# Optimization experiments

Hardware: AMD Instinct MI355X
Metric: run time of the kernel (lower is better)

Reference implementation:

```python
import jax, jax.numpy as jnp
import numpy as np

C_Z = 128
C_HIDDEN = 128
N_RES = 384
B = 1
EPS = 1e-5


def _layernorm(x, w, b):
    mu = jnp.mean(x, axis=-1, keepdims=True)
    var = jnp.mean(jnp.square(x - mu), axis=-1, keepdims=True)
    return (x - mu) * jax.lax.rsqrt(var + EPS) * w + b


def setup_inputs() -> dict:
    key = jax.random.key(0)
    ks = jax.random.split(key, 16)
    s_z = 1.0 / np.sqrt(C_Z)
    s_h = 1.0 / np.sqrt(C_HIDDEN)
    return {
        "z": jax.random.normal(ks[0], (B, N_RES, N_RES, C_Z), dtype=jnp.float32),
        "mask": jnp.ones((B, N_RES, N_RES), dtype=jnp.float32),
        "ln_in_w": jnp.ones((C_Z,), jnp.float32),
        "ln_in_b": jnp.zeros((C_Z,), jnp.float32),
        "a_g_w": jax.random.normal(ks[1], (C_HIDDEN, C_Z), jnp.float32) * s_z,
        "a_g_b": jnp.zeros((C_HIDDEN,), jnp.float32),
        "a_p_w": jax.random.normal(ks[2], (C_HIDDEN, C_Z), jnp.float32) * s_z,
        "a_p_b": jnp.zeros((C_HIDDEN,), jnp.float32),
        "b_g_w": jax.random.normal(ks[3], (C_HIDDEN, C_Z), jnp.float32) * s_z,
        "b_g_b": jnp.zeros((C_HIDDEN,), jnp.float32),
        "b_p_w": jax.random.normal(ks[4], (C_HIDDEN, C_Z), jnp.float32) * s_z,
        "b_p_b": jnp.zeros((C_HIDDEN,), jnp.float32),
        "g_w": jax.random.normal(ks[5], (C_Z, C_Z), jnp.float32) * s_z,
        "g_b": jnp.zeros((C_Z,), jnp.float32),
        "ln_out_w": jnp.ones((C_HIDDEN,), jnp.float32),
        "ln_out_b": jnp.zeros((C_HIDDEN,), jnp.float32),
        "z_w": jax.random.normal(ks[6], (C_Z, C_HIDDEN), jnp.float32) * s_h,
        "z_b": jnp.zeros((C_Z,), jnp.float32),
    }


def reference(z, mask, ln_in_w, ln_in_b, a_g_w, a_g_b, a_p_w, a_p_b,
              b_g_w, b_g_b, b_p_w, b_p_b, g_w, g_b,
              ln_out_w, ln_out_b, z_w, z_b):
    # z: [B, N, N, c_z]; mask: [B, N, N]
    m = mask[..., None]
    zn = _layernorm(z, ln_in_w, ln_in_b)
    # gated projections (fused LN+GEMM+sigmoid*mul in the Triton kernel)
    a = m * jax.nn.sigmoid(jnp.einsum("bijc,hc->bijh", zn, a_g_w) + a_g_b) \
          * (jnp.einsum("bijc,hc->bijh", zn, a_p_w) + a_p_b)
    b = m * jax.nn.sigmoid(jnp.einsum("bijc,hc->bijh", zn, b_g_w) + b_g_b) \
          * (jnp.einsum("bijc,hc->bijh", zn, b_p_w) + b_p_b)
    # outgoing triangle update: contract over third node k, per channel
    x = jnp.einsum("bikh,bjkh->bijh", a, b)
    # output path: sigmoid(gate(zn)) * linear_z(LN_out(x))
    xn = _layernorm(x, ln_out_w, ln_out_b)
    gate = jax.nn.sigmoid(jnp.einsum("bijc,oc->bijo", zn, g_w) + g_b)
    out = gate * (jnp.einsum("bijh,oh->bijo", xn, z_w) + z_b)
    return out
```

## Files before the change

kernel.cpp:

```cpp
#include <hip/hip_runtime.h>

#define NRES 384
#define CD   128
#define MTOT (NRES*NRES)

typedef unsigned short u16;
typedef __bf16 bf16x8 __attribute__((ext_vector_type(8)));
typedef float  f32x16 __attribute__((ext_vector_type(16)));

static __device__ __forceinline__ u16 f2bf(float f) {
  __bf16 b = (__bf16)f;
  return __builtin_bit_cast(u16, b);
}
static __device__ __forceinline__ float bf2f(u16 v) {
  return __uint_as_float(((unsigned)v) << 16);
}
static __device__ __forceinline__ float sigmoidf(float x) {
  return __builtin_amdgcn_rcpf(1.0f + __expf(-x));
}

static __device__ __forceinline__ void gl16(const void* g, void* l) {
  __builtin_amdgcn_global_load_lds(
      (const __attribute__((address_space(1))) void*)g,
      (__attribute__((address_space(3))) void*)l, 16, 0, 0);
}

__global__ void k_cvt_w(const float* w0, const float* w1, const float* w2,
                        const float* w3, const float* w4, const float* w5,
                        const float* lnw, u16* wb) {
  int i = blockIdx.x * 256 + threadIdx.x;
  int which = blockIdx.x >> 6;
  const float* src = (which == 0) ? w0 : (which == 1) ? w1 : (which == 2) ? w2
                   : (which == 3) ? w3 : (which == 4) ? w4 : w5;
  float v = src[i & 16383];
  if (which == 5) v *= lnw[i & 127];
  wb[i] = f2bf(v);
}

__global__ void k_c12(const float* __restrict__ zw, const float* __restrict__ lnw,
                      const float* __restrict__ lnb, const float* __restrict__ zb,
                      float2* __restrict__ c12) {
  int o = blockIdx.x, l = threadIdx.x;
  float2 v = ((const float2*)(zw + o * CD))[l];
  float2 w = ((const float2*)lnw)[l];
  float2 b = ((const float2*)lnb)[l];
  float s1 = v.x * w.x + v.y * w.y;
  float s2 = v.x * b.x + v.y * b.y;
#pragma unroll
  for (int off = 32; off >= 1; off >>= 1) {
    s1 += __shfl_xor(s1, off);
    s2 += __shfl_xor(s2, off);
  }
  if (l == 0) c12[o] = make_float2(s1, s2 + zb[o]);
}

__global__ __launch_bounds__(256) void k_ln_in(const float* __restrict__ z,
                                               const float* __restrict__ w,
                                               const float* __restrict__ b,
                                               u16* __restrict__ zn) {
  int wv = threadIdx.x >> 6, lane = threadIdx.x & 63;
  float2 wv2 = ((const float2*)w)[lane];
  float2 bv2 = ((const float2*)b)[lane];
  for (int rr = 0; rr < 4; ++rr) {
    size_t row = (size_t)blockIdx.x * 16 + wv * 4 + rr;
    float2 v = ((const float2*)(z + row * CD))[lane];
    float s = v.x + v.y;
#pragma unroll
    for (int off = 32; off >= 1; off >>= 1) s += __shfl_xor(s, off);
    float mu = s * (1.0f / CD);
    float dx = v.x - mu, dy = v.y - mu;
    float vr = dx * dx + dy * dy;
#pragma unroll
    for (int off = 32; off >= 1; off >>= 1) vr += __shfl_xor(vr, off);
    float rs = rsqrtf(vr * (1.0f / CD) + 1e-5f);
    ushort2 o;
    o.x = f2bf(dx * rs * wv2.x + bv2.x);
    o.y = f2bf(dy * rs * wv2.y + bv2.y);
    ((ushort2*)(zn + row * CD))[lane] = o;
  }
}

__global__ __launch_bounds__(256) void k_proj(
    const u16* __restrict__ zn, const float* __restrict__ mask,
    const u16* __restrict__ wb,
    const float* __restrict__ agb, const float* __restrict__ apb,
    const float* __restrict__ bgb, const float* __restrict__ bpb,
    u16* __restrict__ a_out, u16* __restrict__ b_out) {
  int type = blockIdx.y;
  int m_base = blockIdx.x * 256;
  int t = threadIdx.x;
  int lane = t & 63;
  int wvu = __builtin_amdgcn_readfirstlane(t >> 6);
  int nl = lane & 31, s = lane >> 5;
  int h = wvu * 32 + nl;

  const u16* wgp = wb + (size_t)type * 32768;
  const u16* wpp = wgp + 16384;
  const float* bgp = (type == 0) ? agb : bgb;
  const float* bpp = (type == 0) ? apb : bpb;
  u16* outp = (type == 0) ? a_out : b_out;

  __shared__ u16 znt[3][64][128];
  __shared__ float bsl[2][128];

  if (t < 128) bsl[0][t] = bgp[t];
  else         bsl[1][t - 128] = bpp[t - 128];

  float mk0[4], mk1[4];
#pragma unroll
  for (int ms = 0; ms < 4; ++ms) {
    mk0[ms] = mask[m_base + ms * 64 + nl];
    mk1[ms] = mask[m_base + ms * 64 + 32 + nl];
  }

  bf16x8 wgf[8], wpf[8];
#pragma unroll
  for (int kk = 0; kk < 8; ++kk) {
    wgf[kk] = *(const bf16x8*)(wgp + h * CD + kk * 16 + s * 8);
    wpf[kk] = *(const bf16x8*)(wpp + h * CD + kk * 16 + s * 8);
  }

  int rl = lane >> 4, p16 = lane & 15;
#define STAGE_ZNT(mt, bf)                                                   \
  {                                                                         \
    _Pragma("unroll")                                                       \
    for (int j = 0; j < 4; ++j) {                                           \
      int row = wvu * 16 + j * 4 + rl;                                      \
      int gc = (p16 ^ (row & 15)) << 3;                                     \
      gl16(zn + (size_t)((mt) + row) * CD + gc, &znt[bf][wvu * 16 + j * 4][0]); \
    }                                                                       \
  }

  asm volatile("" ::: "memory");
  STAGE_ZNT(m_base, 0);
  asm volatile("" ::: "memory");
  STAGE_ZNT(m_base + 64, 1);
  asm volatile("" ::: "memory");

  asm volatile("s_waitcnt lgkmcnt(0)" ::: "memory");

#define PROJ_ITER(ms, buf, WAITINSN, STAGEIT, stbuf)                          \
  {                                                                           \
    asm volatile(WAITINSN ::: "memory");                                      \
    __builtin_amdgcn_s_barrier();                                             \
    asm volatile("" ::: "memory");                                            \
    f32x16 accg0, accg1, accp0, accp1;                                        \
    _Pragma("unroll")                                                         \
    for (int i = 0; i < 16; ++i) {                                            \
      accg0[i] = 0; accg1[i] = 0; accp0[i] = 0; accp1[i] = 0;                 \
    }                                                                         \
    _Pragma("unroll")                                                         \
    for (int kk = 0; kk < 8; ++kk) {                                          \
      int c = ((kk * 2 + s) ^ (nl & 15)) << 3;                                \
      bf16x8 zf0 = *(const bf16x8*)&znt[buf][nl][c];                          \
      bf16x8 zf1 = *(const bf16x8*)&znt[buf][32 + nl][c];                     \
      accg0 = __builtin_amdgcn_mfma_f32_32x32x16_bf16(wgf[kk], zf0, accg0, 0, 0, 0); \
      accg1 = __builtin_amdgcn_mfma_f32_32x32x16_bf16(wgf[kk], zf1, accg1, 0, 0, 0); \
      accp0 = __builtin_amdgcn_mfma_f32_32x32x16_bf16(wpf[kk], zf0, accp0, 0, 0, 0); \
      accp1 = __builtin_amdgcn_mfma_f32_32x32x16_bf16(wpf[kk], zf1, accp1, 0, 0, 0); \
    }                                                                         \
    int mt = m_base + (ms) * 64;                                              \
    _Pragma("unroll")                                                         \
    for (int r = 0; r < 16; ++r) {                                            \
      int hh = wvu * 32 + (r & 3) + 8 * (r >> 2) + 4 * s;                     \
      float bg = bsl[0][hh], bp = bsl[1][hh];                                 \
      u16* rowp = outp + (size_t)hh * MTOT + mt + nl;                         \
      rowp[0]  = f2bf(mk0[ms] * sigmoidf(accg0[r] + bg) * (accp0[r] + bp));   \
      rowp[32] = f2bf(mk1[ms] * sigmoidf(accg1[r] + bg) * (accp1[r] + bp));   \
    }                                                                         \
    asm volatile("" ::: "memory");                                            \
    if (STAGEIT) STAGE_ZNT(m_base + ((ms) + 2) * 64, stbuf);                  \
    asm volatile("" ::: "memory");                                            \
  }

  PROJ_ITER(0, 0, "s_waitcnt vmcnt(4)",  1, 2);
  PROJ_ITER(1, 1, "s_waitcnt vmcnt(36)", 1, 0);
  PROJ_ITER(2, 2, "s_waitcnt vmcnt(36)", 0, 0);
  PROJ_ITER(3, 0, "s_waitcnt vmcnt(32)", 0, 0);
#undef PROJ_ITER
#undef STAGE_ZNT
}

__global__ __launch_bounds__(256) void k_tri(const u16* __restrict__ a,
                                             const u16* __restrict__ b,
                                             u16* __restrict__ x) {
  int n = blockIdx.x;
  int w = (n & 7) * 144 + (n >> 3);
  int h = w / 9;
  int tile = w % 9;
  int tm = tile / 3, tn = tile % 3;
  int i0 = tm * 128, j0 = tn * 128;
  const u16* ah = a + (size_t)h * MTOT;
  const u16* bh = b + (size_t)h * MTOT;

  __shared__ u16 At[2][128][64];
  __shared__ u16 Bt[2][128][64];

  int lane = threadIdx.x & 63;
  int wvu = __builtin_amdgcn_readfirstlane(threadIdx.x >> 6);
  int nl = lane & 31, s = lane >> 5;
  int wr = wvu >> 1, wc = wvu & 1;
  int rl = lane >> 3, p8 = lane & 7;

  f32x16 acc[4];
#pragma unroll
  for (int q = 0; q < 4; ++q)
#pragma unroll
    for (int i = 0; i < 16; ++i) acc[q][i] = 0;

#define STAGE_TRI(bf, k0)                                                     \
  {                                                                           \
    _Pragma("unroll")                                                         \
    for (int j = 0; j < 4; ++j) {                                             \
      int row = wvu * 32 + j * 8 + rl;                                        \
      int gc = (p8 ^ (rl & 7)) << 3;                                          \
      gl16(ah + (size_t)(i0 + row) * NRES + (k0) + gc, &At[bf][wvu * 32 + j * 8][0]); \
      gl16(bh + (size_t)(j0 + row) * NRES + (k0) + gc, &Bt[bf][wvu * 32 + j * 8][0]); \
    }                                                                         \
  }

  STAGE_TRI(0, 0);
  __syncthreads();

  for (int kb = 0; kb < 6; ++kb) {
    int cur = kb & 1;
    if (kb < 5) STAGE_TRI(cur ^ 1, (kb + 1) * 64);
#pragma unroll
    for (int kk = 0; kk < 4; ++kk) {
      int c = ((kk * 2 + s) ^ (nl & 7)) << 3;
      bf16x8 af0 = *(const bf16x8*)&At[cur][wr * 64 + nl][c];
      bf16x8 af1 = *(const bf16x8*)&At[cur][wr * 64 + 32 + nl][c];
      bf16x8 bf0 = *(const bf16x8*)&Bt[cur][wc * 64 + nl][c];
      bf16x8 bf1 = *(const bf16x8*)&Bt[cur][wc * 64 + 32 + nl][c];
      acc[0] = __builtin_amdgcn_mfma_f32_32x32x16_bf16(af0, bf0, acc[0], 0, 0, 0);
      acc[1] = __builtin_amdgcn_mfma_f32_32x32x16_bf16(af0, bf1, acc[1], 0, 0, 0);
      acc[2] = __builtin_amdgcn_mfma_f32_32x32x16_bf16(af1, bf0, acc[2], 0, 0, 0);
      acc[3] = __builtin_amdgcn_mfma_f32_32x32x16_bf16(af1, bf1, acc[3], 0, 0, 0);
    }
    __syncthreads();
  }
#undef STAGE_TRI

  u16* xh = x + (size_t)h * MTOT;
#pragma unroll
  for (int msub = 0; msub < 2; ++msub)
#pragma unroll
    for (int nsub = 0; nsub < 2; ++nsub) {
      int j = j0 + wc * 64 + nsub * 32 + nl;
#pragma unroll
      for (int r = 0; r < 16; ++r) {
        int i = i0 + wr * 64 + msub * 32 + (r & 3) + 8 * (r >> 2) + 4 * s;
        xh[(size_t)i * NRES + j] = f2bf(acc[msub * 2 + nsub][r]);
      }
    }
}

__global__ __launch_bounds__(256) void k_out(
    const u16* __restrict__ x, const u16* __restrict__ zn,
    const u16* __restrict__ wb, const float* __restrict__ gb,
    const float2* __restrict__ c12, float* __restrict__ out) {
  int m0 = blockIdx.x * 64;
  int t = threadIdx.x;
  int wv = t >> 6, lane = t & 63, nl = lane & 31, s = lane >> 5;
  int o = wv * 32 + nl;

  __shared__ u16 tile[64][136];
  __shared__ float2 stat[64];

  const u16* gwp = wb + 4 * 16384;
  const u16* zwp = wb + 5 * 16384;

  uint4 znv[4];
#pragma unroll
  for (int it = 0; it < 4; ++it) {
    int idx = it * 256 + t, r = idx >> 4, c8 = idx & 15;
    znv[it] = *(const uint4*)(zn + (size_t)(m0 + r) * CD + c8 * 8);
  }
  bf16x8 gwf[8];
#pragma unroll
  for (int kk = 0; kk < 8; ++kk)
    gwf[kk] = *(const bf16x8*)(gwp + o * CD + kk * 16 + s * 8);
  float gbv = gb[o];

  int mc = t & 7;
  uint4 xv0[2], xv1[2];
#pragma unroll
  for (int ps = 0; ps < 2; ++ps) {
    int hp = (ps * 256 + t) >> 3;
    xv0[ps] = *(const uint4*)(x + (size_t)(2 * hp)     * MTOT + m0 + mc * 8);
    xv1[ps] = *(const uint4*)(x + (size_t)(2 * hp + 1) * MTOT + m0 + mc * 8);
  }

#pragma unroll
  for (int it = 0; it < 4; ++it) {
    int idx = it * 256 + t, r = idx >> 4, c8 = idx & 15;
    *(uint4*)&tile[r][c8 * 8] = znv[it];
  }
  asm volatile("s_waitcnt lgkmcnt(0)" ::: "memory");
  __builtin_amdgcn_s_barrier();

  f32x16 gacc[2];
#pragma unroll
  for (int i = 0; i < 16; ++i) { gacc[0][i] = 0; gacc[1][i] = 0; }
#pragma unroll
  for (int kk = 0; kk < 8; ++kk) {
    bf16x8 zf0 = *(const bf16x8*)&tile[nl][kk * 16 + s * 8];
    bf16x8 zf1 = *(const bf16x8*)&tile[32 + nl][kk * 16 + s * 8];
    gacc[0] = __builtin_amdgcn_mfma_f32_32x32x16_bf16(zf0, gwf[kk], gacc[0], 0, 0, 0);
    gacc[1] = __builtin_amdgcn_mfma_f32_32x32x16_bf16(zf1, gwf[kk], gacc[1], 0, 0, 0);
  }
  float gv[32];
#pragma unroll
  for (int ms = 0; ms < 2; ++ms)
#pragma unroll
    for (int r = 0; r < 16; ++r)
      gv[ms * 16 + r] = sigmoidf(gacc[ms][r] + gbv);
  asm volatile("s_waitcnt lgkmcnt(0)" ::: "memory");
  __builtin_amdgcn_s_barrier();

  bf16x8 zwf[8];
#pragma unroll
  for (int kk = 0; kk < 8; ++kk)
    zwf[kk] = *(const bf16x8*)(zwp + o * CD + kk * 16 + s * 8);

#pragma unroll
  for (int ps = 0; ps < 2; ++ps) {
    int hp = (ps * 256 + t) >> 3;
    unsigned c0[4] = {xv0[ps].x, xv0[ps].y, xv0[ps].z, xv0[ps].w};
    unsigned c1[4] = {xv1[ps].x, xv1[ps].y, xv1[ps].z, xv1[ps].w};
#pragma unroll
    for (int q = 0; q < 4; ++q) {
      ushort2 lo, hi;
      lo.x = (u16)(c0[q] & 0xffffu); lo.y = (u16)(c1[q] & 0xffffu);
      hi.x = (u16)(c0[q] >> 16);     hi.y = (u16)(c1[q] >> 16);
      *(ushort2*)&tile[mc * 8 + 2 * q][2 * hp]     = lo;
      *(ushort2*)&tile[mc * 8 + 2 * q + 1][2 * hp] = hi;
    }
  }
  asm volatile("s_waitcnt lgkmcnt(0)" ::: "memory");
  __builtin_amdgcn_s_barrier();

  {
    int r = t >> 2, q = t & 3;
    float sum = 0.0f, sq = 0.0f;
#pragma unroll
    for (int i = 0; i < 4; ++i) {
      uint4 v = *(const uint4*)&tile[r][q * 32 + i * 8];
      unsigned cc[4] = {v.x, v.y, v.z, v.w};
#pragma unroll
      for (int j = 0; j < 4; ++j) {
        float a = bf2f((u16)(cc[j] & 0xffffu));
        float b = bf2f((u16)(cc[j] >> 16));
        sum += a + b; sq += a * a + b * b;
      }
    }
    sum += __shfl_xor(sum, 1); sum += __shfl_xor(sum, 2);
    sq  += __shfl_xor(sq, 1);  sq  += __shfl_xor(sq, 2);
    float mu = sum * (1.0f / CD);
    float var = sq * (1.0f / CD) - mu * mu;
    float rs = rsqrtf(var + 1e-5f);
    if (q == 0) stat[r] = make_float2(rs, rs * mu);
  }

  f32x16 acc[2];
#pragma unroll
  for (int i = 0; i < 16; ++i) { acc[0][i] = 0; acc[1][i] = 0; }
#pragma unroll
  for (int kk = 0; kk < 8; ++kk) {
    bf16x8 af0 = *(const bf16x8*)&tile[nl][kk * 16 + s * 8];
    bf16x8 af1 = *(const bf16x8*)&tile[32 + nl][kk * 16 + s * 8];
    acc[0] = __builtin_amdgcn_mfma_f32_32x32x16_bf16(af0, zwf[kk], acc[0], 0, 0, 0);
    acc[1] = __builtin_amdgcn_mfma_f32_32x32x16_bf16(af1, zwf[kk], acc[1], 0, 0, 0);
  }
  asm volatile("s_waitcnt lgkmcnt(0)" ::: "memory");
  __builtin_amdgcn_s_barrier();

  float2 cc2 = c12[o];
#pragma unroll
  for (int ms = 0; ms < 2; ++ms)
#pragma unroll
    for (int rr = 0; rr < 16; ++rr) {
      int rowoff = (rr & 3) + 8 * (rr >> 2) + 4 * s;
      int row = ms * 32 + rowoff;
      float2 st = stat[row];
      out[(size_t)(m0 + row) * CD + o] =
          gv[ms * 16 + rr] * (st.x * acc[ms][rr] - st.y * cc2.x + cc2.y);
    }
}

extern "C" void kernel_launch(void* const* d_in, const int* in_sizes, int n_in,
                              void* d_out, int out_size, void* d_ws, size_t ws_size,
                              hipStream_t stream) {
  const float* z       = (const float*)d_in[0];
  const float* mask    = (const float*)d_in[1];
  const float* ln_in_w = (const float*)d_in[2];
  const float* ln_in_b = (const float*)d_in[3];
  const float* a_g_w   = (const float*)d_in[4];
  const float* a_g_b   = (const float*)d_in[5];
  const float* a_p_w   = (const float*)d_in[6];
  const float* a_p_b   = (const float*)d_in[7];
  const float* b_g_w   = (const float*)d_in[8];
  const float* b_g_b   = (const float*)d_in[9];
  const float* b_p_w   = (const float*)d_in[10];
  const float* b_p_b   = (const float*)d_in[11];
  const float* g_w     = (const float*)d_in[12];
  const float* g_b     = (const float*)d_in[13];
  const float* ln_o_w  = (const float*)d_in[14];
  const float* ln_o_b  = (const float*)d_in[15];
  const float* z_w     = (const float*)d_in[16];
  const float* z_b     = (const float*)d_in[17];
  float* out = (float*)d_out;

  const size_t SZ = (size_t)MTOT * CD * sizeof(u16);
  char* w = (char*)d_ws;
  u16* zn = (u16*)(w);
  u16* a  = (u16*)(w + SZ);
  u16* b  = (u16*)(w + 2 * SZ);
  u16* x  = (u16*)(w + 3 * SZ);
  u16* wb = (u16*)(w + 4 * SZ);
  float2* c12 = (float2*)(w + 4 * SZ + 6 * 16384 * sizeof(u16));
  (void)ws_size; (void)in_sizes; (void)n_in; (void)out_size;

  k_cvt_w<<<384, 256, 0, stream>>>(a_g_w, a_p_w, b_g_w, b_p_w, g_w, z_w,
                                   ln_o_w, wb);
  k_c12<<<128, 64, 0, stream>>>(z_w, ln_o_w, ln_o_b, z_b, c12);
  k_ln_in<<<MTOT / 16, 256, 0, stream>>>(z, ln_in_w, ln_in_b, zn);
  k_proj<<<dim3(MTOT / 256, 2), 256, 0, stream>>>(zn, mask, wb,
      a_g_b, a_p_b, b_g_b, b_p_b, a, b);
  k_tri<<<1152, 256, 0, stream>>>(a, b, x);
  k_out<<<MTOT / 64, 256, 0, stream>>>(x, zn, wb, g_b, c12, out);
}
```

Measured before the change: 261.6 us.

## Replace syncthreads loop with counted-vmcnt prefetch pipeline in triangle GEMM; shrink projection LDS

The triangle-multiply kernel now runs a fully unrolled two-deep prefetch pipeline that waits on explicit vmcnt counts and raw s_barrier. This replaces the __syncthreads loop, which drained all outstanding loads every iteration. The projection kernel drops from three to two LDS stage buffers and adds an extra barrier before refilling a buffer. That cuts shared memory use, which may raise occupancy, but adds synchronization and less prefetch depth.

```diff
diff --git a/kernel.cpp b/kernel.cpp
--- a/kernel.cpp
+++ b/kernel.cpp
@@ -100,7 +100,7 @@
   const float* bpp = (type == 0) ? apb : bpb;
   u16* outp = (type == 0) ? a_out : b_out;
 
-  __shared__ u16 znt[3][64][128];
+  __shared__ u16 znt[2][64][128];
   __shared__ float bsl[2][128];
 
   if (t < 128) bsl[0][t] = bgp[t];
@@ -139,7 +139,7 @@
 
   asm volatile("s_waitcnt lgkmcnt(0)" ::: "memory");
 
-#define PROJ_ITER(ms, buf, WAITINSN, STAGEIT, stbuf)                          \
+#define PROJ_ITER(ms, buf, WAITINSN, STAGEIT)                                 \
   {                                                                           \
     asm volatile(WAITINSN ::: "memory");                                      \
     __builtin_amdgcn_s_barrier();                                             \
@@ -169,14 +169,18 @@
       rowp[32] = f2bf(mk1[ms] * sigmoidf(accg1[r] + bg) * (accp1[r] + bp));   \
     }                                                                         \
     asm volatile("" ::: "memory");                                            \
-    if (STAGEIT) STAGE_ZNT(m_base + ((ms) + 2) * 64, stbuf);                  \
-    asm volatile("" ::: "memory");                                            \
-  }
-
-  PROJ_ITER(0, 0, "s_waitcnt vmcnt(4)",  1, 2);
-  PROJ_ITER(1, 1, "s_waitcnt vmcnt(36)", 1, 0);
-  PROJ_ITER(2, 2, "s_waitcnt vmcnt(36)", 0, 0);
-  PROJ_ITER(3, 0, "s_waitcnt vmcnt(32)", 0, 0);
+    if (STAGEIT) {                                                            \
+      __builtin_amdgcn_s_barrier();        \
+      asm volatile("" ::: "memory");                                          \
+      STAGE_ZNT(m_base + ((ms) + 2) * 64, buf);                               \
+      asm volatile("" ::: "memory");                                          \
+    }                                                                         \
+  }
+
+  PROJ_ITER(0, 0, "s_waitcnt vmcnt(4)",  1);
+  PROJ_ITER(1, 1, "s_waitcnt vmcnt(36)", 1);
+  PROJ_ITER(2, 0, "s_waitcnt vmcnt(36)", 0);
+  PROJ_ITER(3, 1, "s_waitcnt vmcnt(32)", 0);
 #undef PROJ_ITER
 #undef STAGE_ZNT
 }
@@ -219,26 +223,46 @@
     }                                                                         \
   }
 
+  asm volatile("" ::: "memory");
   STAGE_TRI(0, 0);
-  __syncthreads();
-
-  for (int kb = 0; kb < 6; ++kb) {
-    int cur = kb & 1;
-    if (kb < 5) STAGE_TRI(cur ^ 1, (kb + 1) * 64);
-#pragma unroll
-    for (int kk = 0; kk < 4; ++kk) {
-      int c = ((kk * 2 + s) ^ (nl & 7)) << 3;
-      bf16x8 af0 = *(const bf16x8*)&At[cur][wr * 64 + nl][c];
-      bf16x8 af1 = *(const bf16x8*)&At[cur][wr * 64 + 32 + nl][c];
-      bf16x8 bf0 = *(const bf16x8*)&Bt[cur][wc * 64 + nl][c];
-      bf16x8 bf1 = *(const bf16x8*)&Bt[cur][wc * 64 + 32 + nl][c];
-      acc[0] = __builtin_amdgcn_mfma_f32_32x32x16_bf16(af0, bf0, acc[0], 0, 0, 0);
-      acc[1] = __builtin_amdgcn_mfma_f32_32x32x16_bf16(af0, bf1, acc[1], 0, 0, 0);
-      acc[2] = __builtin_amdgcn_mfma_f32_32x32x16_bf16(af1, bf0, acc[2], 0, 0, 0);
-      acc[3] = __builtin_amdgcn_mfma_f32_32x32x16_bf16(af1, bf1, acc[3], 0, 0, 0);
-    }
-    __syncthreads();
-  }
+  asm volatile("" ::: "memory");
+  STAGE_TRI(1, 64);
+  asm volatile("" ::: "memory");
+
+#define TRI_ITER(kb, WAITINSN, STAGEIT)                                       \
+  {                                                                           \
+    const int cur = (kb) & 1;                                                 \
+    asm volatile(WAITINSN ::: "memory");                                      \
+    __builtin_amdgcn_s_barrier();                                             \
+    asm volatile("" ::: "memory");                                            \
+    _Pragma("unroll")                                                         \
+    for (int kk = 0; kk < 4; ++kk) {                                          \
+      int c = ((kk * 2 + s) ^ (nl & 7)) << 3;                                 \
+      bf16x8 af0 = *(const bf16x8*)&At[cur][wr * 64 + nl][c];                 \
+      bf16x8 af1 = *(const bf16x8*)&At[cur][wr * 64 + 32 + nl][c];            \
+      bf16x8 bf0 = *(const bf16x8*)&Bt[cur][wc * 64 + nl][c];                 \
+      bf16x8 bf1 = *(const bf16x8*)&Bt[cur][wc * 64 + 32 + nl][c];            \
+      acc[0] = __builtin_amdgcn_mfma_f32_32x32x16_bf16(af0, bf0, acc[0], 0, 0, 0); \
+      acc[1] = __builtin_amdgcn_mfma_f32_32x32x16_bf16(af0, bf1, acc[1], 0, 0, 0); \
+      acc[2] = __builtin_amdgcn_mfma_f32_32x32x16_bf16(af1, bf0, acc[2], 0, 0, 0); \
+      acc[3] = __builtin_amdgcn_mfma_f32_32x32x16_bf16(af1, bf1, acc[3], 0, 0, 0); \
+    }                                                                         \
+    asm volatile("s_waitcnt lgkmcnt(0)" ::: "memory");                        \
+    if (STAGEIT) {                                                            \
+      __builtin_amdgcn_s_barrier();        \
+      asm volatile("" ::: "memory");                                          \
+      STAGE_TRI(cur, ((kb) + 2) * 64);                                        \
+      asm volatile("" ::: "memory");                                          \
+    }                                                                         \
+  }
+
+  TRI_ITER(0, "s_waitcnt vmcnt(8)", 1);
+  TRI_ITER(1, "s_waitcnt vmcnt(8)", 1);
+  TRI_ITER(2, "s_waitcnt vmcnt(8)", 1);
+  TRI_ITER(3, "s_waitcnt vmcnt(8)", 1);
+  TRI_ITER(4, "s_waitcnt vmcnt(8)", 0);
+  TRI_ITER(5, "s_waitcnt vmcnt(0)", 0);
+#undef TRI_ITER
 #undef STAGE_TRI
 
   u16* xh = x + (size_t)h * MTOT;
```

Measured after the change: 274.5 us. 1.05x slower.
